# Performance work log

Measured on AMD Instinct MI355X. Metric: run time of the kernel, lower is better.

The kernel has to match this reference:

```python
import jax, jax.numpy as jnp
import numpy as np

B, T, DM, DF, E, K = 4, 1024, 768, 3072, 8, 2


def setup_inputs() -> dict:
    key = jax.random.key(0)
    k0, k1, k2, k3 = jax.random.split(key, 4)
    x = jax.random.normal(k0, (B, T, DM), jnp.float32)
    Wg = jax.random.normal(k1, (DM, E), jnp.float32) * 0.02
    W1 = jax.random.normal(k2, (E, DM, DF), jnp.float32) * 0.02
    b1 = jnp.zeros((E, DF), jnp.float32)
    W2 = jax.random.normal(k3, (E, DF, DM), jnp.float32) * 0.02
    b2 = jnp.zeros((E, DM), jnp.float32)
    return {"x": x, "Wg": Wg, "W1": W1, "b1": b1, "W2": W2, "b2": b2}


def reference(x, Wg, W1, b1, W2, b2):
    # --- flatten (s)equence x (t)oken -> S tokens of width m ---
    m = x.shape[-1]
    xs = x.reshape(-1, m)              # [S, m]
    S = xs.shape[0]
    n_exp = W1.shape[0]

    # --- top-k softmax gate: combine_weights [k,S], dispatch order sorted by expert ---
    logits = xs @ Wg                   # [S, E]
    probs = jax.nn.softmax(logits, axis=-1)
    topv, topi = jax.lax.top_k(probs, K)                 # [S, K]
    cw = topv / jnp.sum(topv, axis=-1, keepdims=True)    # renormalize top-k
    combine_weights = cw.T                               # [K, S]

    # slot layout: slot = j*S + s (matches rerouted_output.reshape(k, S, m))
    eid_flat = topi.T.reshape(-1)                        # [S*K] expert id per slot
    dispatch_mask = jnp.argsort(eid_flat)                # stable sort by expert == chunked order
    e_sorted = eid_flat[dispatch_mask]                   # [S*K] sorted expert ids

    # --- dispatch: gather token rows (dispatch_mask % S indexes the token) ---
    dispatched = xs[dispatch_mask % S]                   # [S*K, m]

    # --- experts: per-expert FFN; loop over fixed small expert count, masked combine ---
    expert_outputs = jnp.zeros_like(dispatched)
    for e in range(n_exp):
        sel = (e_sorted == e)[:, None].astype(dispatched.dtype)
        h = jax.nn.relu(dispatched @ W1[e] + b1[e])      # [S*K, DF]
        expert_outputs = expert_outputs + sel * (h @ W2[e] + b2[e])

    # --- scatter back to slot order, then weighted combine over k ---
    rerouted = jnp.zeros((S * K, m), expert_outputs.dtype).at[dispatch_mask].set(expert_outputs)
    rerouted = rerouted.reshape(K, S, m)
    combined = jnp.einsum('ks,ksm->sm', combine_weights, rerouted)
    return combined.reshape(x.shape).astype(x.dtype)
```

## Files before the change

### kernel.cpp

```cpp
#include <hip/hip_runtime.h>
#include <math.h>

typedef short short8 __attribute__((ext_vector_type(8)));
typedef float f32x4 __attribute__((ext_vector_type(4)));
typedef unsigned short u16;
typedef unsigned int u32;

#define S_TOK 4096
#define DM 768
#define DF 3072
#define NE 8
#define NSLOT (S_TOK*2)
#define PSLOT 9216
#define MBMAX 72

#define WS_COUNTS   0
#define WS_CURSOR   512
#define WS_OFFS     1024
#define WS_MBE      1088
#define WS_EID      2048
#define WS_GW       (WS_EID + NSLOT*4)
#define WS_POS      (WS_GW  + NSLOT*4)
#define WS_TOK      (WS_POS + NSLOT*4)
#define CTRL_BYTES  262144

#define AS1 __attribute__((address_space(1)))
#define AS3 __attribute__((address_space(3)))
#define GLDS16(g, s) __builtin_amdgcn_global_load_lds((const AS1 u32*)(g), (AS3 u32*)(s), 16, 0, 0)

__device__ inline u16 f2b(float f){
    u32 u = __builtin_bit_cast(u32, f);
    u32 r = (u + 0x7fffu + ((u >> 16) & 1u)) >> 16;
    return (u16)r;
}
__device__ inline short8 ldcvt8f(const float* p){
    float4 a = *(const float4*)p;
    float4 b = *(const float4*)(p + 4);
    short8 v;
    v[0]=(short)f2b(a.x); v[1]=(short)f2b(a.y); v[2]=(short)f2b(a.z); v[3]=(short)f2b(a.w);
    v[4]=(short)f2b(b.x); v[5]=(short)f2b(b.y); v[6]=(short)f2b(b.z); v[7]=(short)f2b(b.w);
    return v;
}

#define GATE_BLOCKS 128
__global__ __launch_bounds__(256) void gate_kernel(const float* __restrict__ x, const float* __restrict__ Wg,
                                                   int* __restrict__ eid, float* __restrict__ gw,
                                                   int* __restrict__ counts){
    __shared__ int lh[NE];
    int t = threadIdx.x;
    if (t < NE) lh[t] = 0;
    __syncthreads();
    int wv = t >> 6, l = t & 63;
    int wgid = blockIdx.x*4 + wv;
    const int NW = GATE_BLOCKS*4;

    for (int s = wgid; s < S_TOK; s += NW){
        float acc[NE];
#pragma unroll
        for (int e = 0; e < NE; e++) acc[e] = 0.f;
        const float* xr = x + (size_t)s * DM;
#pragma unroll
        for (int i = 0; i < DM/64; i++){
            int d = l + 64*i;
            float xv = xr[d];
            float4 w0 = *(const float4*)(Wg + d*NE);
            float4 w1 = *(const float4*)(Wg + d*NE + 4);
            acc[0] += xv*w0.x; acc[1] += xv*w0.y; acc[2] += xv*w0.z; acc[3] += xv*w0.w;
            acc[4] += xv*w1.x; acc[5] += xv*w1.y; acc[6] += xv*w1.z; acc[7] += xv*w1.w;
        }
#pragma unroll
        for (int e = 0; e < NE; e++){
#pragma unroll
            for (int off = 32; off; off >>= 1) acc[e] += __shfl_down(acc[e], off);
        }
        if (l == 0){
            int i1 = 0; float v1 = acc[0];
            for (int e = 1; e < NE; e++) if (acc[e] > v1){ v1 = acc[e]; i1 = e; }
            int i2 = -1; float v2 = -1e30f;
            for (int e = 0; e < NE; e++) if (e != i1 && acc[e] > v2){ v2 = acc[e]; i2 = e; }
            float w0, w1;
            if (i2 < 0){ i2 = (i1 + 1) & 7; w0 = 1.f; w1 = 0.f; }
            else {
                float e2 = expf(v2 - v1);
                w0 = 1.f / (1.f + e2);
                w1 = e2 / (1.f + e2);
            }
            eid[2*s]   = i1; gw[2*s]   = w0;
            eid[2*s+1] = i2; gw[2*s+1] = w1;
            atomicAdd(&lh[i1], 1);
            atomicAdd(&lh[i2], 1);
        }
    }
    __syncthreads();
    if (t < NE && lh[t] > 0) atomicAdd(&counts[t*16], lh[t]);
}

__global__ void offsets_kernel(const int* __restrict__ counts, int* __restrict__ offs,
                               int* __restrict__ cursor, int* __restrict__ mbe){
    if (threadIdx.x == 0 && blockIdx.x == 0){
        int P = 0;
        for (int e = 0; e < NE; e++){
            offs[e] = P; cursor[e*16] = P;
            int padded = ((counts[e*16] + 127) >> 7) << 7;
            for (int mb = P >> 7; mb < (P + padded) >> 7; mb++) mbe[mb] = e;
            P += padded;
        }
        offs[NE] = P;
        for (int mb = P >> 7; mb < MBMAX; mb++) mbe[mb] = -1;
    }
}

__global__ __launch_bounds__(256) void scatter_kernel(const int* __restrict__ eid, int* __restrict__ cursor,
                                                      const int* __restrict__ counts, const int* __restrict__ offs,
                                                      const int* __restrict__ mbe,
                                                      int* __restrict__ tok_of, int* __restrict__ pos_of){
    __shared__ int lh[NE];
    __shared__ int base[NE];
    int t = threadIdx.x;
    if (t < NE) lh[t] = 0;
    __syncthreads();
    int i = blockIdx.x*256 + t;
    int e = 0, r = 0;
    if (i < NSLOT){
        e = eid[i];
        if (e < 0) e = 0; if (e > 7) e = 7;
        r = atomicAdd(&lh[e], 1);
    }
    __syncthreads();
    if (t < NE) base[t] = (lh[t] > 0) ? atomicAdd(&cursor[t*16], lh[t]) : 0;
    __syncthreads();
    if (i < NSLOT){
        int p = base[e] + r;
        if (p < 0) p = 0; if (p >= PSLOT) p = PSLOT - 1;
        tok_of[p] = i >> 1;
        pos_of[i] = p;
    }
    int p = i;
    int pe = mbe[p >> 7];
    if (pe < 0){ tok_of[p] = 0; }
    else if (p >= offs[pe] + counts[pe*16]){ tok_of[p] = 0; }
}

__global__ __launch_bounds__(256) void cvtx_kernel(const float* __restrict__ x, u16* __restrict__ xb,
                                                   int* __restrict__ counts, int* __restrict__ cursor){
    if (blockIdx.x == 0 && threadIdx.x < 128){ counts[threadIdx.x] = 0; cursor[threadIdx.x] = 0; }
    int i = (blockIdx.x*256 + threadIdx.x)*8;
    *(short8*)&xb[i] = ldcvt8f(&x[i]);
}

__global__ __launch_bounds__(256) void cvtshuf_kernel(const float* __restrict__ W, u16* __restrict__ Ws,
                                                      int Kd, int Nd){
    int kbn = Kd >> 5;
    int kb = blockIdx.x % kbn;
    int nb = blockIdx.x / kbn;
    int e  = blockIdx.y;
    const float* Wp = W + (size_t)e * Kd * Nd;
    u16* Wsp       = Ws + (size_t)e * Kd * Nd;
    int t = threadIdx.x;
    __shared__ u16 sh[32*136];
#pragma unroll
    for (int i = 0; i < 2; i++){
        int c = t + 256*i;
        int k = c >> 4, nc = c & 15;
        *(short8*)&sh[k*136 + nc*8] = ldcvt8f(&Wp[(size_t)(kb*32 + k)*Nd + nb*128 + nc*8]);
    }
    __syncthreads();
    int w = t >> 6, l = t & 63;
#pragma unroll
    for (int o = 0; o < 2; o++){
        int nt = 2*w + o;
        int n = nt*16 + (l & 15);
        short8 v;
#pragma unroll
        for (int j = 0; j < 8; j++) v[j] = (short)sh[((l >> 4)*8 + j)*136 + n];
        *(short8*)&Wsp[(size_t)(((nb*8 + nt) * kbn + kb) * 512) + l*8] = v;
    }
}

__global__ __launch_bounds__(256) void gemm1u_kernel(const u16* __restrict__ xb, const int* __restrict__ tok_of,
                                                     const int* __restrict__ mbe, const u16* __restrict__ W1s,
                                                     const float* __restrict__ b1, u16* __restrict__ h){
    const int KB = DM/32;
    const int KB2 = DM/64;
    int bid = blockIdx.x;
    int by = bid % 24, mb = bid / 24;
    int e = mbe[mb];
    if (e < 0) return;
    int m0 = mb*128, n0 = by*128;

    int t = threadIdx.x;
    int w = t >> 6, l = t & 63;
    int wm = w & 1, wn = w >> 1;

    __shared__ u16 As[128*72];
    __shared__ u16 Bs[2*2*8*512];

    int row0 = t >> 2, kc = t & 3;
    const u16* a0 = xb + (size_t)tok_of[m0 + row0]*DM + kc*8;
    const u16* a1 = xb + (size_t)tok_of[m0 + row0 + 64]*DM + kc*8;
    u16* as0 = &As[row0*72 + kc*8];
    u16* as1 = &As[(row0 + 64)*72 + kc*8];

    const u16* bbase = W1s + (size_t)e*DM*DF + (size_t)(((n0 >> 4) + 2*w)*KB)*512 + l*8;

    f32x4 acc[4][4];
#pragma unroll
    for (int i = 0; i < 4; i++)
#pragma unroll
        for (int j = 0; j < 4; j++) acc[i][j] = (f32x4){0.f,0.f,0.f,0.f};

    {
        short8 p0 = *(const short8*)a0;
        short8 p1 = *(const short8*)(a0 + 32);
        short8 p2 = *(const short8*)a1;
        short8 p3 = *(const short8*)(a1 + 32);
        *(short8*)as0 = p0; *(short8*)(as0 + 32) = p1;
        *(short8*)as1 = p2; *(short8*)(as1 + 32) = p3;
        GLDS16(bbase,                            &Bs[(2*w)*512]);
        GLDS16(bbase + 512,                      &Bs[4096 + (2*w)*512]);
        GLDS16(bbase + (size_t)KB*512,           &Bs[(2*w+1)*512]);
        GLDS16(bbase + (size_t)KB*512 + 512,     &Bs[4096 + (2*w+1)*512]);
    }
    __syncthreads();

    int c = 0;
    short8 av0a, av0b, av1a, av1b;
    for (int kb2 = 0; kb2 < KB2; kb2++){
        if (kb2 + 1 < KB2){
            GLDS16(bbase + (size_t)(2*kb2+2)*512,                     &Bs[(c^1)*8192 + (2*w)*512]);
            GLDS16(bbase + (size_t)(2*kb2+3)*512,                     &Bs[(c^1)*8192 + 4096 + (2*w)*512]);
            GLDS16(bbase + (size_t)KB*512 + (size_t)(2*kb2+2)*512,    &Bs[(c^1)*8192 + (2*w+1)*512]);
            GLDS16(bbase + (size_t)KB*512 + (size_t)(2*kb2+3)*512,    &Bs[(c^1)*8192 + 4096 + (2*w+1)*512]);
            av0a = *(const short8*)(a0 + (kb2+1)*64);
            av0b = *(const short8*)(a0 + (kb2+1)*64 + 32);
            av1a = *(const short8*)(a1 + (kb2+1)*64);
            av1b = *(const short8*)(a1 + (kb2+1)*64 + 32);
        }
#pragma unroll
        for (int ks = 0; ks < 2; ks++){
            short8 af[4], bf[4];
#pragma unroll
            for (int mt = 0; mt < 4; mt++)
                af[mt] = *(const short8*)&As[(wm*64 + mt*16 + (l & 15))*72 + ks*32 + (l >> 4)*8];
#pragma unroll
            for (int nt = 0; nt < 4; nt++)
                bf[nt] = *(const short8*)&Bs[c*8192 + ks*4096 + (wn*4 + nt)*512 + l*8];
#pragma unroll
            for (int mt = 0; mt < 4; mt++)
#pragma unroll
                for (int nt = 0; nt < 4; nt++)
                    acc[mt][nt] = __builtin_amdgcn_mfma_f32_16x16x32_bf16(af[mt], bf[nt], acc[mt][nt], 0, 0, 0);
        }
        __syncthreads();
        if (kb2 + 1 < KB2){
            *(short8*)as0 = av0a; *(short8*)(as0 + 32) = av0b;
            *(short8*)as1 = av1a; *(short8*)(as1 + 32) = av1b;
            __syncthreads();
        }
        c ^= 1;
    }

#pragma unroll
    for (int nt = 0; nt < 4; nt++){
        int col = n0 + wn*64 + nt*16 + (l & 15);
        float bv = b1[e*DF + col];
#pragma unroll
        for (int mt = 0; mt < 4; mt++){
#pragma unroll
            for (int r = 0; r < 4; r++){
                int grow = m0 + wm*64 + mt*16 + (l >> 4)*4 + r;
                float v = acc[mt][nt][r] + bv;
                v = v > 0.f ? v : 0.f;
                h[(size_t)grow*DF + col] = f2b(v);
            }
        }
    }
}

__global__ __launch_bounds__(256) void gemm2p_kernel(const u16* __restrict__ h, const int* __restrict__ mbe,
                                                     const u16* __restrict__ W2s, const float* __restrict__ b2,
                                                     float* __restrict__ y){
    const int KB = DF/32;
    const int NT = DF/64;
    int bid = blockIdx.x;
    int mb = bid % MBMAX;
    int by = bid / MBMAX;
    int e = mbe[mb];
    if (e < 0) return;
    int m0 = mb*128, n0 = by*128;

    int t = threadIdx.x;
    int w = t >> 6, l = t & 63;
    int wm = w & 1, wn = w >> 1;

    __shared__ u16 As[128*72];
    __shared__ u16 Bs[3*2*8*512];

    int row0 = t >> 2, kc = t & 3;
    const u16* a0 = h + (size_t)(m0 + row0)*DF + kc*8;
    const u16* a1 = h + (size_t)(m0 + row0 + 64)*DF + kc*8;
    u16* as0 = &As[row0*72 + kc*8];
    u16* as1 = &As[(row0 + 64)*72 + kc*8];

    const u16* bbase = W2s + (size_t)e*DF*DM + (size_t)(((n0 >> 4) + 2*w)*KB)*512 + l*8;

#define STB2(kb2, buf) do{ \
    GLDS16(bbase + (size_t)(2*(kb2))*512,                   &Bs[(buf)*8192 + (2*w)*512]); \
    GLDS16(bbase + (size_t)(2*(kb2)+1)*512,                 &Bs[(buf)*8192 + 4096 + (2*w)*512]); \
    GLDS16(bbase + (size_t)KB*512 + (size_t)(2*(kb2))*512,  &Bs[(buf)*8192 + (2*w+1)*512]); \
    GLDS16(bbase + (size_t)KB*512 + (size_t)(2*(kb2)+1)*512,&Bs[(buf)*8192 + 4096 + (2*w+1)*512]); \
}while(0)

    f32x4 acc[4][4];
#pragma unroll
    for (int i = 0; i < 4; i++)
#pragma unroll
        for (int j = 0; j < 4; j++) acc[i][j] = (f32x4){0.f,0.f,0.f,0.f};

    short8 av0a = *(const short8*)a0;
    short8 av0b = *(const short8*)(a0 + 32);
    short8 av1a = *(const short8*)a1;
    short8 av1b = *(const short8*)(a1 + 32);
    STB2(0, 0);
    STB2(1, 1);
    *(short8*)as0 = av0a; *(short8*)(as0 + 32) = av0b;
    *(short8*)as1 = av1a; *(short8*)(as1 + 32) = av1b;
    av0a = *(const short8*)(a0 + 64);
    av0b = *(const short8*)(a0 + 96);
    av1a = *(const short8*)(a1 + 64);
    av1b = *(const short8*)(a1 + 96);
    __builtin_amdgcn_sched_barrier(0);
    asm volatile("s_waitcnt vmcnt(8) lgkmcnt(0)" ::: "memory");
    __builtin_amdgcn_sched_barrier(0);
    __builtin_amdgcn_s_barrier();

    int cb = 0, sb = 2;
    for (int kt = 0; kt < NT; kt++){
        if (kt + 2 < NT) STB2(kt + 2, sb);
#pragma unroll
        for (int ks = 0; ks < 2; ks++){
            short8 af[4], bf[4];
#pragma unroll
            for (int mt = 0; mt < 4; mt++)
                af[mt] = *(const short8*)&As[(wm*64 + mt*16 + (l & 15))*72 + ks*32 + (l >> 4)*8];
#pragma unroll
            for (int nt = 0; nt < 4; nt++)
                bf[nt] = *(const short8*)&Bs[cb*8192 + ks*4096 + (wn*4 + nt)*512 + l*8];
#pragma unroll
            for (int mt = 0; mt < 4; mt++)
#pragma unroll
                for (int nt = 0; nt < 4; nt++)
                    acc[mt][nt] = __builtin_amdgcn_mfma_f32_16x16x32_bf16(af[mt], bf[nt], acc[mt][nt], 0, 0, 0);
        }
        __builtin_amdgcn_sched_barrier(0);
        asm volatile("s_waitcnt vmcnt(4) lgkmcnt(0)" ::: "memory");
        __builtin_amdgcn_sched_barrier(0);
        __builtin_amdgcn_s_barrier();
        if (kt + 1 < NT){
            *(short8*)as0 = av0a; *(short8*)(as0 + 32) = av0b;
            *(short8*)as1 = av1a; *(short8*)(as1 + 32) = av1b;
            if (kt + 2 < NT){
                av0a = *(const short8*)(a0 + (kt+2)*64);
                av0b = *(const short8*)(a0 + (kt+2)*64 + 32);
                av1a = *(const short8*)(a1 + (kt+2)*64);
                av1b = *(const short8*)(a1 + (kt+2)*64 + 32);
            }
            __builtin_amdgcn_sched_barrier(0);
            asm volatile("s_waitcnt lgkmcnt(0)" ::: "memory");
            __builtin_amdgcn_sched_barrier(0);
            __builtin_amdgcn_s_barrier();
        }
        cb = (cb == 2) ? 0 : cb + 1;
        sb = (sb == 2) ? 0 : sb + 1;
    }
#undef STB2

#pragma unroll
    for (int nt = 0; nt < 4; nt++){
        int col = n0 + wn*64 + nt*16 + (l & 15);
        float bv = b2[e*DM + col];
#pragma unroll
        for (int mt = 0; mt < 4; mt++){
#pragma unroll
            for (int r = 0; r < 4; r++){
                int grow = m0 + wm*64 + mt*16 + (l >> 4)*4 + r;
                y[(size_t)grow*DM + col] = acc[mt][nt][r] + bv;
            }
        }
    }
}

__global__ __launch_bounds__(256) void combine_kernel(const float* __restrict__ y, const int* __restrict__ pos_of,
                                                      const float* __restrict__ gw, float* __restrict__ out){
    int i = blockIdx.x*256 + threadIdx.x;
    int s = i / (DM/4);
    int c4 = (i - s*(DM/4))*4;
    int p0 = pos_of[2*s], p1 = pos_of[2*s+1];
    float w0 = gw[2*s], w1 = gw[2*s+1];
    float4 a = *(const float4*)&y[(size_t)p0*DM + c4];
    float4 b = *(const float4*)&y[(size_t)p1*DM + c4];
    float4 o;
    o.x = w0*a.x + w1*b.x;
    o.y = w0*a.y + w1*b.y;
    o.z = w0*a.z + w1*b.z;
    o.w = w0*a.w + w1*b.w;
    *(float4*)&out[(size_t)s*DM + c4] = o;
}

__global__ __launch_bounds__(256) void fallback_kernel(const float* __restrict__ x, const float* __restrict__ Wg,
                                                       const float* __restrict__ W1, const float* __restrict__ b1,
                                                       const float* __restrict__ W2, const float* __restrict__ b2,
                                                       float* __restrict__ out){
    int s = blockIdx.x;
    int t = threadIdx.x;
    __shared__ float xr[DM];
    __shared__ float hl[DF];
    __shared__ float yl[DM];
    __shared__ float lacc[4*NE];
    __shared__ int   sel_e[2];
    __shared__ float sel_w[2];

    for (int i = t; i < DM; i += 256){ xr[i] = x[(size_t)s*DM + i]; yl[i] = 0.f; }
    __syncthreads();

    float acc[NE];
#pragma unroll
    for (int e = 0; e < NE; e++) acc[e] = 0.f;
    for (int d = t*3; d < t*3 + 3; d++){
        float xv = xr[d];
#pragma unroll
        for (int e = 0; e < NE; e++) acc[e] += xv * Wg[d*NE + e];
    }
#pragma unroll
    for (int e = 0; e < NE; e++){
#pragma unroll
        for (int off = 32; off; off >>= 1) acc[e] += __shfl_down(acc[e], off);
    }
    if ((t & 63) == 0){
        int wv = t >> 6;
#pragma unroll
        for (int e = 0; e < NE; e++) lacc[wv*NE + e] = acc[e];
    }
    __syncthreads();
    if (t == 0){
        float lg[NE];
#pragma unroll
        for (int e = 0; e < NE; e++) lg[e] = lacc[e] + lacc[NE + e] + lacc[2*NE + e] + lacc[3*NE + e];
        int i1 = 0; float v1 = lg[0];
        for (int e = 1; e < NE; e++) if (lg[e] > v1){ v1 = lg[e]; i1 = e; }
        int i2 = -1; float v2 = -1e30f;
        for (int e = 0; e < NE; e++) if (e != i1 && lg[e] > v2){ v2 = lg[e]; i2 = e; }
        if (i2 < 0){ i2 = (i1 + 1) & 7; sel_w[0] = 1.f; sel_w[1] = 0.f; }
        else {
            float e2 = expf(v2 - v1);
            sel_w[0] = 1.f / (1.f + e2);
            sel_w[1] = e2 / (1.f + e2);
        }
        sel_e[0] = i1; sel_e[1] = i2;
    }
    __syncthreads();

    for (int kk = 0; kk < 2; kk++){
        int e = sel_e[kk];
        float wgt = sel_w[kk];
        const float* w1p = W1 + (size_t)e * DM * DF;
        for (int j = t; j < DF; j += 256){
            float a = b1[e*DF + j];
            for (int k = 0; k < DM; k++) a += xr[k] * w1p[(size_t)k*DF + j];
            hl[j] = a > 0.f ? a : 0.f;
        }
        __syncthreads();
        const float* w2p = W2 + (size_t)e * DF * DM;
        for (int c = t; c < DM; c += 256){
            float a = b2[e*DM + c];
            for (int k = 0; k < DF; k++) a += hl[k] * w2p[(size_t)k*DM + c];
            yl[c] += wgt * a;
        }
        __syncthreads();
    }
    for (int c = t; c < DM; c += 256) out[(size_t)s*DM + c] = yl[c];
}

extern "C" void kernel_launch(void* const* d_in, const int* in_sizes, int n_in,
                              void* d_out, int out_size, void* d_ws, size_t ws_size,
                              hipStream_t stream) {
    const float* x  = (const float*)d_in[0];
    const float* Wg = (const float*)d_in[1];
    const float* W1 = (const float*)d_in[2];
    const float* b1 = (const float*)d_in[3];
    const float* W2 = (const float*)d_in[4];
    const float* b2 = (const float*)d_in[5];
    float* out = (float*)d_out;

    char* ws = (char*)d_ws;
    int*   counts = (int*)(ws + WS_COUNTS);
    int*   cursor = (int*)(ws + WS_CURSOR);
    int*   offs   = (int*)(ws + WS_OFFS);
    int*   mbe    = (int*)(ws + WS_MBE);
    int*   eid    = (int*)(ws + WS_EID);
    float* gw     = (float*)(ws + WS_GW);
    int*   pos_of = (int*)(ws + WS_POS);
    int*   tok_of = (int*)(ws + WS_TOK);

    const size_t xbB = (size_t)S_TOK*DM*2;
    const size_t wB  = (size_t)NE*DM*DF*2;
    const size_t hB  = (size_t)PSLOT*DF*2;
    const size_t need = CTRL_BYTES + xbB + 2*wB + hB;

    if (ws_size < need){
        fallback_kernel<<<S_TOK, 256, 0, stream>>>(x, Wg, W1, b1, W2, b2, out);
        return;
    }

    u16* xb  = (u16*)(ws + CTRL_BYTES);
    u16* W1s = (u16*)(ws + CTRL_BYTES + xbB);
    u16* W2s = (u16*)(ws + CTRL_BYTES + xbB + wB);
    u16* h   = (u16*)(ws + CTRL_BYTES + xbB + 2*wB);
    float* yb = (float*)(ws + CTRL_BYTES + xbB);

    cvtx_kernel<<<S_TOK*DM/8/256, 256, 0, stream>>>(x, xb, counts, cursor);
    cvtshuf_kernel<<<dim3((DM/32)*(DF/128), NE), 256, 0, stream>>>(W1, W1s, DM, DF);
    cvtshuf_kernel<<<dim3((DF/32)*(DM/128), NE), 256, 0, stream>>>(W2, W2s, DF, DM);
    gate_kernel<<<GATE_BLOCKS, 256, 0, stream>>>(x, Wg, eid, gw, counts);
    offsets_kernel<<<1, 1, 0, stream>>>(counts, offs, cursor, mbe);
    scatter_kernel<<<PSLOT/256, 256, 0, stream>>>(eid, cursor, counts, offs, mbe, tok_of, pos_of);

    gemm1u_kernel<<<MBMAX*24, 256, 0, stream>>>(xb, tok_of, mbe, W1s, b1, h);
    gemm2p_kernel<<<6*MBMAX, 256, 0, stream>>>(h, mbe, W2s, b2, yb);
    combine_kernel<<<(S_TOK*(DM/4))/256, 256, 0, stream>>>(yb, pos_of, gw, out);
}
```

Before: 345.7 us.

## Merge weight conversions into one kernel, fold x conversion into gate, deepen GEMM1 prefetch

The two weight convert-and-shuffle launches become a single kernel that does the transpose through strided global loads instead of shared memory. The separate x-to-bf16 kernel is removed, and the gate kernel writes the bf16 copy of x as it reads x. GEMM1's main loop now prefetches A rows two steps ahead and replaces __syncthreads with explicit vmcnt waits plus s_barrier, so B's async LDS loads can stay in flight across the barrier. The strided weight reads and scalar 2-byte xb stores may lower memory efficiency, and the hand-written waitcnt counts have to match the actual number of outstanding loads to stay correct.

```diff
diff --git a/kernel.cpp b/kernel.cpp
--- a/kernel.cpp
+++ b/kernel.cpp
@@ -33,19 +33,46 @@
     u32 r = (u + 0x7fffu + ((u >> 16) & 1u)) >> 16;
     return (u16)r;
 }
-__device__ inline short8 ldcvt8f(const float* p){
-    float4 a = *(const float4*)p;
-    float4 b = *(const float4*)(p + 4);
-    short8 v;
-    v[0]=(short)f2b(a.x); v[1]=(short)f2b(a.y); v[2]=(short)f2b(a.z); v[3]=(short)f2b(a.w);
-    v[4]=(short)f2b(b.x); v[5]=(short)f2b(b.y); v[6]=(short)f2b(b.z); v[7]=(short)f2b(b.w);
-    return v;
+
+__global__ __launch_bounds__(256) void cvtw_kernel(const float* __restrict__ W1, u16* __restrict__ W1s,
+                                                   const float* __restrict__ W2, u16* __restrict__ W2s,
+                                                   int* __restrict__ counts, int* __restrict__ cursor){
+    if (blockIdx.x == 0 && blockIdx.y == 0 && threadIdx.x < 128){
+        counts[threadIdx.x] = 0; cursor[threadIdx.x] = 0;
+    }
+    int e = blockIdx.y;
+    int b = blockIdx.x;
+    const float* Wp; u16* Wsp; int Kd, Nd;
+    if (b < 576){ Wp = W1; Wsp = W1s; Kd = DM; Nd = DF; }
+    else        { b -= 576; Wp = W2; Wsp = W2s; Kd = DF; Nd = DM; }
+    int kbn = Kd >> 5;
+    Wp  += (size_t)e*Kd*Nd;
+    Wsp += (size_t)e*Kd*Nd;
+    int t = threadIdx.x;
+    int u = b*256 + t;
+    int l   = u & 63;
+    int kb  = (u >> 6) % kbn;
+    int qq  = (u >> 6) / kbn;
+    int ntp = qq & 3;
+    int nb  = qq >> 2;
+    int k0 = kb*32 + (l >> 4)*8;
+    int c  = nb*128 + ntp*32 + (l & 15);
+    const float* src = Wp + (size_t)k0*Nd + c;
+    short8 o0, o1;
+#pragma unroll
+    for (int j = 0; j < 8; j++){
+        o0[j] = (short)f2b(src[(size_t)j*Nd]);
+        o1[j] = (short)f2b(src[(size_t)j*Nd + 16]);
+    }
+    size_t v0 = ((size_t)(nb*8 + ntp*2)*kbn + kb)*64 + l;
+    *(short8*)&Wsp[v0*8] = o0;
+    *(short8*)&Wsp[v0*8 + (size_t)kbn*512] = o1;
 }
 
 #define GATE_BLOCKS 128
 __global__ __launch_bounds__(256) void gate_kernel(const float* __restrict__ x, const float* __restrict__ Wg,
                                                    int* __restrict__ eid, float* __restrict__ gw,
-                                                   int* __restrict__ counts){
+                                                   int* __restrict__ counts, u16* __restrict__ xb){
     __shared__ int lh[NE];
     int t = threadIdx.x;
     if (t < NE) lh[t] = 0;
@@ -59,10 +86,12 @@
 #pragma unroll
         for (int e = 0; e < NE; e++) acc[e] = 0.f;
         const float* xr = x + (size_t)s * DM;
+        u16* xbr = xb + (size_t)s * DM;
 #pragma unroll
         for (int i = 0; i < DM/64; i++){
             int d = l + 64*i;
             float xv = xr[d];
+            xbr[d] = f2b(xv);
             float4 w0 = *(const float4*)(Wg + d*NE);
             float4 w1 = *(const float4*)(Wg + d*NE + 4);
             acc[0] += xv*w0.x; acc[1] += xv*w0.y; acc[2] += xv*w0.z; acc[3] += xv*w0.w;
@@ -141,47 +170,11 @@
     else if (p >= offs[pe] + counts[pe*16]){ tok_of[p] = 0; }
 }
 
-__global__ __launch_bounds__(256) void cvtx_kernel(const float* __restrict__ x, u16* __restrict__ xb,
-                                                   int* __restrict__ counts, int* __restrict__ cursor){
-    if (blockIdx.x == 0 && threadIdx.x < 128){ counts[threadIdx.x] = 0; cursor[threadIdx.x] = 0; }
-    int i = (blockIdx.x*256 + threadIdx.x)*8;
-    *(short8*)&xb[i] = ldcvt8f(&x[i]);
-}
-
-__global__ __launch_bounds__(256) void cvtshuf_kernel(const float* __restrict__ W, u16* __restrict__ Ws,
-                                                      int Kd, int Nd){
-    int kbn = Kd >> 5;
-    int kb = blockIdx.x % kbn;
-    int nb = blockIdx.x / kbn;
-    int e  = blockIdx.y;
-    const float* Wp = W + (size_t)e * Kd * Nd;
-    u16* Wsp       = Ws + (size_t)e * Kd * Nd;
-    int t = threadIdx.x;
-    __shared__ u16 sh[32*136];
-#pragma unroll
-    for (int i = 0; i < 2; i++){
-        int c = t + 256*i;
-        int k = c >> 4, nc = c & 15;
-        *(short8*)&sh[k*136 + nc*8] = ldcvt8f(&Wp[(size_t)(kb*32 + k)*Nd + nb*128 + nc*8]);
-    }
-    __syncthreads();
-    int w = t >> 6, l = t & 63;
-#pragma unroll
-    for (int o = 0; o < 2; o++){
-        int nt = 2*w + o;
-        int n = nt*16 + (l & 15);
-        short8 v;
-#pragma unroll
-        for (int j = 0; j < 8; j++) v[j] = (short)sh[((l >> 4)*8 + j)*136 + n];
-        *(short8*)&Wsp[(size_t)(((nb*8 + nt) * kbn + kb) * 512) + l*8] = v;
-    }
-}
-
-__global__ __launch_bounds__(256) void gemm1u_kernel(const u16* __restrict__ xb, const int* __restrict__ tok_of,
+__global__ __launch_bounds__(256) void gemm1p_kernel(const u16* __restrict__ xb, const int* __restrict__ tok_of,
                                                      const int* __restrict__ mbe, const u16* __restrict__ W1s,
                                                      const float* __restrict__ b1, u16* __restrict__ h){
     const int KB = DM/32;
-    const int KB2 = DM/64;
+    const int NT = DM/64;
     int bid = blockIdx.x;
     int by = bid % 24, mb = bid / 24;
     int e = mbe[mb];
@@ -203,39 +196,38 @@
 
     const u16* bbase = W1s + (size_t)e*DM*DF + (size_t)(((n0 >> 4) + 2*w)*KB)*512 + l*8;
 
+#define STB1(kb2, buf) do{ \
+    GLDS16(bbase + (size_t)(2*(kb2))*512,                   &Bs[(buf)*8192 + (2*w)*512]); \
+    GLDS16(bbase + (size_t)(2*(kb2)+1)*512,                 &Bs[(buf)*8192 + 4096 + (2*w)*512]); \
+    GLDS16(bbase + (size_t)KB*512 + (size_t)(2*(kb2))*512,  &Bs[(buf)*8192 + (2*w+1)*512]); \
+    GLDS16(bbase + (size_t)KB*512 + (size_t)(2*(kb2)+1)*512,&Bs[(buf)*8192 + 4096 + (2*w+1)*512]); \
+}while(0)
+
     f32x4 acc[4][4];
 #pragma unroll
     for (int i = 0; i < 4; i++)
 #pragma unroll
         for (int j = 0; j < 4; j++) acc[i][j] = (f32x4){0.f,0.f,0.f,0.f};
 
-    {
-        short8 p0 = *(const short8*)a0;
-        short8 p1 = *(const short8*)(a0 + 32);
-        short8 p2 = *(const short8*)a1;
-        short8 p3 = *(const short8*)(a1 + 32);
-        *(short8*)as0 = p0; *(short8*)(as0 + 32) = p1;
-        *(short8*)as1 = p2; *(short8*)(as1 + 32) = p3;
-        GLDS16(bbase,                            &Bs[(2*w)*512]);
-        GLDS16(bbase + 512,                      &Bs[4096 + (2*w)*512]);
-        GLDS16(bbase + (size_t)KB*512,           &Bs[(2*w+1)*512]);
-        GLDS16(bbase + (size_t)KB*512 + 512,     &Bs[4096 + (2*w+1)*512]);
-    }
-    __syncthreads();
-
-    int c = 0;
-    short8 av0a, av0b, av1a, av1b;
-    for (int kb2 = 0; kb2 < KB2; kb2++){
-        if (kb2 + 1 < KB2){
-            GLDS16(bbase + (size_t)(2*kb2+2)*512,                     &Bs[(c^1)*8192 + (2*w)*512]);
-            GLDS16(bbase + (size_t)(2*kb2+3)*512,                     &Bs[(c^1)*8192 + 4096 + (2*w)*512]);
-            GLDS16(bbase + (size_t)KB*512 + (size_t)(2*kb2+2)*512,    &Bs[(c^1)*8192 + (2*w+1)*512]);
-            GLDS16(bbase + (size_t)KB*512 + (size_t)(2*kb2+3)*512,    &Bs[(c^1)*8192 + 4096 + (2*w+1)*512]);
-            av0a = *(const short8*)(a0 + (kb2+1)*64);
-            av0b = *(const short8*)(a0 + (kb2+1)*64 + 32);
-            av1a = *(const short8*)(a1 + (kb2+1)*64);
-            av1b = *(const short8*)(a1 + (kb2+1)*64 + 32);
-        }
+    short8 av0a = *(const short8*)a0;
+    short8 av0b = *(const short8*)(a0 + 32);
+    short8 av1a = *(const short8*)a1;
+    short8 av1b = *(const short8*)(a1 + 32);
+    STB1(0, 0);
+    *(short8*)as0 = av0a; *(short8*)(as0 + 32) = av0b;
+    *(short8*)as1 = av1a; *(short8*)(as1 + 32) = av1b;
+    av0a = *(const short8*)(a0 + 64);
+    av0b = *(const short8*)(a0 + 96);
+    av1a = *(const short8*)(a1 + 64);
+    av1b = *(const short8*)(a1 + 96);
+    __builtin_amdgcn_sched_barrier(0);
+    asm volatile("s_waitcnt vmcnt(4) lgkmcnt(0)" ::: "memory");
+    __builtin_amdgcn_sched_barrier(0);
+    __builtin_amdgcn_s_barrier();
+
+    int cb = 0;
+    for (int kt = 0; kt < NT; kt++){
+        if (kt + 1 < NT) STB1(kt + 1, cb ^ 1);
 #pragma unroll
         for (int ks = 0; ks < 2; ks++){
             short8 af[4], bf[4];
@@ -244,21 +236,38 @@
                 af[mt] = *(const short8*)&As[(wm*64 + mt*16 + (l & 15))*72 + ks*32 + (l >> 4)*8];
 #pragma unroll
             for (int nt = 0; nt < 4; nt++)
-                bf[nt] = *(const short8*)&Bs[c*8192 + ks*4096 + (wn*4 + nt)*512 + l*8];
+                bf[nt] = *(const short8*)&Bs[cb*8192 + ks*4096 + (wn*4 + nt)*512 + l*8];
 #pragma unroll
             for (int mt = 0; mt < 4; mt++)
 #pragma unroll
                 for (int nt = 0; nt < 4; nt++)
                     acc[mt][nt] = __builtin_amdgcn_mfma_f32_16x16x32_bf16(af[mt], bf[nt], acc[mt][nt], 0, 0, 0);
         }
-        __syncthreads();
-        if (kb2 + 1 < KB2){
+        __builtin_amdgcn_sched_barrier(0);
+        asm volatile("s_waitcnt vmcnt(4) lgkmcnt(0)" ::: "memory");
+        __builtin_amdgcn_sched_barrier(0);
+        __builtin_amdgcn_s_barrier();
+        if (kt + 1 < NT){
             *(short8*)as0 = av0a; *(short8*)(as0 + 32) = av0b;
             *(short8*)as1 = av1a; *(short8*)(as1 + 32) = av1b;
-            __syncthreads();
-        }
-        c ^= 1;
-    }
+            if (kt + 2 < NT){
+                av0a = *(const short8*)(a0 + (kt+2)*64);
+                av0b = *(const short8*)(a0 + (kt+2)*64 + 32);
+                av1a = *(const short8*)(a1 + (kt+2)*64);
+                av1b = *(const short8*)(a1 + (kt+2)*64 + 32);
+                __builtin_amdgcn_sched_barrier(0);
+                asm volatile("s_waitcnt vmcnt(4) lgkmcnt(0)" ::: "memory");
+                __builtin_amdgcn_sched_barrier(0);
+            } else {
+                __builtin_amdgcn_sched_barrier(0);
+                asm volatile("s_waitcnt vmcnt(0) lgkmcnt(0)" ::: "memory");
+                __builtin_amdgcn_sched_barrier(0);
+            }
+            __builtin_amdgcn_s_barrier();
+        }
+        cb ^= 1;
+    }
+#undef STB1
 
 #pragma unroll
     for (int nt = 0; nt < 4; nt++){
@@ -518,14 +527,12 @@
     u16* h   = (u16*)(ws + CTRL_BYTES + xbB + 2*wB);
     float* yb = (float*)(ws + CTRL_BYTES + xbB);
 
-    cvtx_kernel<<<S_TOK*DM/8/256, 256, 0, stream>>>(x, xb, counts, cursor);
-    cvtshuf_kernel<<<dim3((DM/32)*(DF/128), NE), 256, 0, stream>>>(W1, W1s, DM, DF);
-    cvtshuf_kernel<<<dim3((DF/32)*(DM/128), NE), 256, 0, stream>>>(W2, W2s, DF, DM);
-    gate_kernel<<<GATE_BLOCKS, 256, 0, stream>>>(x, Wg, eid, gw, counts);
+    cvtw_kernel<<<dim3(1152, NE), 256, 0, stream>>>(W1, W1s, W2, W2s, counts, cursor);
+    gate_kernel<<<GATE_BLOCKS, 256, 0, stream>>>(x, Wg, eid, gw, counts, xb);
     offsets_kernel<<<1, 1, 0, stream>>>(counts, offs, cursor, mbe);
     scatter_kernel<<<PSLOT/256, 256, 0, stream>>>(eid, cursor, counts, offs, mbe, tok_of, pos_of);
 
-    gemm1u_kernel<<<MBMAX*24, 256, 0, stream>>>(xb, tok_of, mbe, W1s, b1, h);
+    gemm1p_kernel<<<MBMAX*24, 256, 0, stream>>>(xb, tok_of, mbe, W1s, b1, h);
     gemm2p_kernel<<<6*MBMAX, 256, 0, stream>>>(h, mbe, W2s, b2, yb);
     combine_kernel<<<(S_TOK*(DM/4))/256, 256, 0, stream>>>(yb, pos_of, gw, out);
 }
```

New measurement: 344.4 us. About the same (-0.4%).
